# Performance work log

Hardware: AMD Instinct MI355X
Metric: run time of the kernel (lower is better)

## Reference

```python
import jax, jax.numpy as jnp
import numpy as np

N_NODES = 200_000
N_EDGES = 6_400_000
N_GRAPHS = 1024
F_IN = 16
H1 = 8
H2 = 16
STEPS = 4


def setup_inputs() -> dict:
    key = jax.random.key(0)
    ks = jax.random.split(key, 16)
    x = jax.random.normal(ks[0], (N_NODES, F_IN), jnp.float32)
    edge_index = jax.random.randint(ks[1], (2, N_EDGES), 0, N_NODES, dtype=jnp.int64)
    batch = jnp.sort(jax.random.randint(ks[2], (N_NODES,), 0, N_GRAPHS, dtype=jnp.int64))

    def p(k, shape):
        return jax.random.normal(k, shape, jnp.float32) * 0.1

    return {
        "x": x, "edge_index": edge_index, "batch": batch,
        # SAGEConv1: lin_l (neighbors, with bias) + lin_r (root, no bias)
        "W1l": p(ks[3], (H1, F_IN)), "b1l": jnp.zeros((H1,), jnp.float32), "W1r": p(ks[4], (H1, F_IN)),
        # SAGEConv2
        "W2l": p(ks[5], (H2, H1)), "b2l": jnp.zeros((H2,), jnp.float32), "W2r": p(ks[6], (H2, H1)),
        # Set2Set LSTM: input 2*H2, hidden H2, torch gate order (i, f, g, o)
        "Wih": p(ks[7], (4 * H2, 2 * H2)), "Whh": p(ks[8], (4 * H2, H2)),
        "bih": jnp.zeros((4 * H2,), jnp.float32), "bhh": jnp.zeros((4 * H2,), jnp.float32),
        # Final fc: 2*H2 -> 2
        "Wfc": p(ks[9], (2, 2 * H2)), "bfc": jnp.zeros((2,), jnp.float32),
    }


def _sage_conv(x, src, dst, Wl, bl, Wr):
    # PyG SAGEConv (mean aggr): out = lin_l(mean_j x_j) + lin_r(x_i)
    n = x.shape[0]
    agg = jax.ops.segment_sum(x[src], dst, num_segments=n)          # [N, F]
    deg = jax.ops.segment_sum(jnp.ones_like(dst, dtype=x.dtype), dst, num_segments=n)
    agg = agg / jnp.maximum(deg, 1.0)[:, None]
    return agg @ Wl.T + bl + x @ Wr.T


def _set2set(x, batch, Wih, Whh, bih, bhh):
    # order-invariant pooling with iterative content attention
    B = N_GRAPHS
    h = jnp.zeros((B, H2), x.dtype)
    c = jnp.zeros((B, H2), x.dtype)
    q_star = jnp.zeros((B, 2 * H2), x.dtype)
    for _ in range(STEPS):
        gates = q_star @ Wih.T + bih + h @ Whh.T + bhh
        i, f, g, o = jnp.split(gates, 4, axis=-1)
        c = jax.nn.sigmoid(f) * c + jax.nn.sigmoid(i) * jnp.tanh(g)
        h = jax.nn.sigmoid(o) * jnp.tanh(c)
        q = h                                                      # [B, H2]
        e = jnp.sum(x * q[batch], axis=-1)                         # [N]
        emax = jax.ops.segment_max(e, batch, num_segments=B)
        a = jnp.exp(e - emax[batch])
        asum = jax.ops.segment_sum(a, batch, num_segments=B)
        a = a / asum[batch]                                        # segment softmax
        r = jax.ops.segment_sum(a[:, None] * x, batch, num_segments=B)  # [B, H2]
        q_star = jnp.concatenate([q, r], axis=-1)
    return q_star


def reference(x, edge_index, batch, W1l, b1l, W1r, W2l, b2l, W2r,
              Wih, Whh, bih, bhh, Wfc, bfc):
    src, dst = edge_index[0], edge_index[1]
    x = jax.nn.relu(_sage_conv(x, src, dst, W1l, b1l, W1r))
    x = jax.nn.relu(_sage_conv(x, src, dst, W2l, b2l, W2r))
    q_star = _set2set(x, batch, Wih, Whh, bih, bhh)
    return q_star @ Wfc.T + bfc
```

## Files before the change

### kernel.cpp

```cpp
#include <hip/hip_runtime.h>

#define N_NODES 200000
#define N_EDGES 6400000
#define N_GRAPHS 1024
#define F_IN 16
#define H1 8
#define H2 16
#define STEPS 4

#define NB 1024
#define BNODES 196
#define NSLAB 8
#define CAPS 1024
#define BSLOTS (NSLAB * CAPS)
#define CAP 8784
#define SMAX 320
#define RPT 16
#define RPADD 200
#define ZIDX N_NODES

typedef _Float16 half8 __attribute__((ext_vector_type(8)));
typedef int int4v __attribute__((ext_vector_type(4)));

__global__ void k_y1(const float* __restrict__ x, const float* __restrict__ W1l,
                     _Float16* __restrict__ y1, _Float16* __restrict__ h1) {
    int n = blockIdx.x * blockDim.x + threadIdx.x;
    if (n > N_NODES) return;
    if (n == N_NODES) {
        half8 z = {};
        *(half8*)&y1[(long long)ZIDX * H1] = z;
        *(half8*)&h1[(long long)ZIDX * H1] = z;
        return;
    }
    float xv[F_IN];
#pragma unroll
    for (int k = 0; k < F_IN; k++) xv[k] = x[(long long)n * F_IN + k];
    half8 o;
#pragma unroll
    for (int j = 0; j < H1; j++) {
        float s = 0.f;
#pragma unroll
        for (int k = 0; k < F_IN; k++) s += W1l[j * F_IN + k] * xv[k];
        o[j] = (_Float16)s;
    }
    *(half8*)&y1[(long long)n * H1] = o;
}

#define FILL_T 16384
__global__ __launch_bounds__(1024) void k_bin_fill(const int* __restrict__ src,
                                                   const int* __restrict__ dst,
                                                   int* __restrict__ gcur8,
                                                   unsigned int* __restrict__ grec) {
    __shared__ int scnt[NB];
    __shared__ int soff[NB];
    int tid = threadIdx.x;
    int slab = blockIdx.x & (NSLAB - 1);
    long long ebase = (long long)blockIdx.x * FILL_T;
    scnt[tid] = 0;
    __syncthreads();
    unsigned int rec[16];
    unsigned int meta[16];
#pragma unroll
    for (int u = 0; u < 16; u++) {
        long long e = ebase + (long long)u * 1024 + tid;
        if (e < N_EDGES) {
            int d = __builtin_nontemporal_load(dst + e);
            int s = __builtin_nontemporal_load(src + e);
            int b = d / BNODES;
            int dl = d - b * BNODES;
            rec[u] = ((unsigned int)s << 8) | (unsigned int)dl;
            int r = atomicAdd(&scnt[b], 1);
            meta[u] = ((unsigned int)b << 16) | (unsigned int)r;
        } else {
            meta[u] = 0xFFFFFFFFu;
        }
    }
    __syncthreads();
    {
        int c = scnt[tid];
        soff[tid] = c ? atomicAdd(&gcur8[tid * NSLAB + slab], c) : 0;
    }
    __syncthreads();
#pragma unroll
    for (int u = 0; u < 16; u++) {
        if (meta[u] != 0xFFFFFFFFu) {
            int b = meta[u] >> 16;
            unsigned int slot = (unsigned int)soff[b] + (meta[u] & 0xFFFFu);
            if (slot < CAPS)
                grec[(size_t)b * BSLOTS + slab * CAPS + slot] = rec[u];
        }
    }
}

__global__ __launch_bounds__(512) void k_conv1(
    const float* __restrict__ x, const _Float16* __restrict__ y1,
    const int* __restrict__ gcur8, unsigned int* __restrict__ grec,
    int* __restrict__ growptr,
    const float* __restrict__ b1l, const float* __restrict__ W1r,
    _Float16* __restrict__ h1) {
    __shared__ __align__(16) int lsrc[CAP];
    __shared__ int hist[BNODES];
    __shared__ int start[BNODES + 1];
    __shared__ int slen[BNODES];
    __shared__ int wsum[8];
    __shared__ int cnt8[NSLAB];
    int b = blockIdx.x, tid = threadIdx.x;
    size_t base = (size_t)b * BSLOTS;
    if (tid < NSLAB) {
        int c = gcur8[b * NSLAB + tid];
        cnt8[tid] = c > CAPS ? CAPS : c;
    }
    for (int j = tid; j < BNODES; j += 512) hist[j] = 0;
    __syncthreads();
    unsigned int rec[RPT];
#pragma unroll
    for (int u = 0; u < RPT; u++) {
        int idx = u * 512 + tid;
        int s = idx >> 10, slot = idx & (CAPS - 1);
        if (slot < cnt8[s]) {
            rec[u] = __builtin_nontemporal_load(grec + base + idx);
            atomicAdd(&hist[rec[u] & 255], 1);
        } else {
            rec[u] = 0xFFFFFFFFu;
        }
    }
    __syncthreads();
    {
        int v = (tid < BNODES) ? hist[tid] : 0;
        int pl = (v + 3) & ~3;
        int lane = tid & 63, w = tid >> 6;
        int s = pl;
#pragma unroll
        for (int off = 1; off < 64; off <<= 1) {
            int u = __shfl_up(s, off);
            if (lane >= off) s += u;
        }
        if (lane == 63) wsum[w] = s;
        __syncthreads();
        int bb = 0;
        for (int i = 0; i < w; i++) bb += wsum[i];
        s += bb;
        int ps = s - pl;
        if (tid < BNODES) {
            start[tid] = ps; slen[tid] = v;
            growptr[b * RPADD + tid] = (ps << 16) | v;
        }
        if (tid == BNODES) {
            start[tid] = ps;
            growptr[b * RPADD + tid] = (ps << 16);
        }
    }
    __syncthreads();
    int ptotal = start[BNODES];
    for (int j = tid; j < BNODES; j += 512) hist[j] = 0;
    for (int j = tid; j < ptotal; j += 512) lsrc[j] = ZIDX;
    __syncthreads();
#pragma unroll
    for (int u = 0; u < RPT; u++) {
        if (rec[u] != 0xFFFFFFFFu) {
            int dl = rec[u] & 255;
            int k = atomicAdd(&hist[dl], 1);
            lsrc[start[dl] + k] = (int)(rec[u] >> 8);
        }
    }
    __syncthreads();
    {
        int pe = ptotal > BSLOTS ? BSLOTS : ptotal;
        for (int j = tid * 4; j < pe; j += 2048) {
            int4v vv = *(const int4v*)&lsrc[j];
            __builtin_nontemporal_store(vv, (int4v*)(grec + base + j));
        }
    }
    if (tid < 2 * BNODES) {
        int dl = tid >> 1, half = tid & 1;
        int n = b * BNODES + dl;
        int ps0 = start[dl];
        int nblk = (start[dl + 1] - ps0) >> 2;
        int c0 = half ? (nblk >> 1) : 0;
        int c1 = half ? nblk : (nblk >> 1);
        float acc[H1];
#pragma unroll
        for (int k = 0; k < H1; k++) acc[k] = 0.f;
        for (int blk = c0; blk < c1; blk++) {
            int4v a = *(const int4v*)&lsrc[ps0 + 4 * blk];
            half8 v0 = *(const half8*)&y1[(long long)a.x * H1];
            half8 v1 = *(const half8*)&y1[(long long)a.y * H1];
            half8 v2 = *(const half8*)&y1[(long long)a.z * H1];
            half8 v3 = *(const half8*)&y1[(long long)a.w * H1];
#pragma unroll
            for (int k = 0; k < H1; k++)
                acc[k] += ((float)v0[k] + (float)v1[k]) + ((float)v2[k] + (float)v3[k]);
        }
#pragma unroll
        for (int k = 0; k < H1; k++) acc[k] += __shfl_xor(acc[k], 1);
        if (half == 0 && n < N_NODES) {
            float inv = 1.0f / fmaxf((float)slen[dl], 1.0f);
            float xv[F_IN];
#pragma unroll
            for (int k = 0; k < F_IN; k++) xv[k] = x[(long long)n * F_IN + k];
            half8 o;
#pragma unroll
            for (int j = 0; j < H1; j++) {
                float s = acc[j] * inv + b1l[j];
#pragma unroll
                for (int k = 0; k < F_IN; k++) s += W1r[j * F_IN + k] * xv[k];
                o[j] = (_Float16)fmaxf(s, 0.0f);
            }
            *(half8*)&h1[(long long)n * H1] = o;
        }
    }
}

__global__ __launch_bounds__(512) void k_conv2(
    const _Float16* __restrict__ h1,
    const unsigned int* __restrict__ gsorted, const int* __restrict__ growptr,
    const float* __restrict__ b2l, const float* __restrict__ W2l,
    const float* __restrict__ W2r, float* __restrict__ h2) {
    int b = blockIdx.x, tid = threadIdx.x;
    if (tid >= 2 * BNODES) return;
    int dl = tid >> 1, half = tid & 1;
    int n = b * BNODES + dl;
    if (n >= N_NODES) return;
    int pack0 = growptr[b * RPADD + dl];
    int pack1 = growptr[b * RPADD + dl + 1];
    int ps0 = pack0 >> 16, sl = pack0 & 0xFFFF;
    int nblk = ((pack1 >> 16) - ps0) >> 2;
    const int4v* seg4 = (const int4v*)(gsorted + (size_t)b * BSLOTS + ps0);
    int c0 = half ? (nblk >> 1) : 0;
    int c1 = half ? nblk : (nblk >> 1);
    float acc[H1];
#pragma unroll
    for (int k = 0; k < H1; k++) acc[k] = 0.f;
    for (int blk = c0; blk < c1; blk++) {
        int4v a = __builtin_nontemporal_load(seg4 + blk);
        half8 v0 = *(const half8*)&h1[(long long)a.x * H1];
        half8 v1 = *(const half8*)&h1[(long long)a.y * H1];
        half8 v2 = *(const half8*)&h1[(long long)a.z * H1];
        half8 v3 = *(const half8*)&h1[(long long)a.w * H1];
#pragma unroll
        for (int k = 0; k < H1; k++)
            acc[k] += ((float)v0[k] + (float)v1[k]) + ((float)v2[k] + (float)v3[k]);
    }
#pragma unroll
    for (int k = 0; k < H1; k++) acc[k] += __shfl_xor(acc[k], 1);
    if (half == 0) {
        float inv = 1.0f / fmaxf((float)sl, 1.0f);
        float av[H1], hv[H1];
        half8 hr = *(const half8*)&h1[(long long)n * H1];
#pragma unroll
        for (int k = 0; k < H1; k++) { hv[k] = (float)hr[k]; av[k] = acc[k] * inv; }
        float o[H2];
#pragma unroll
        for (int j = 0; j < H2; j++) {
            float s = b2l[j];
#pragma unroll
            for (int k = 0; k < H1; k++) s += W2l[j * H1 + k] * av[k] + W2r[j * H1 + k] * hv[k];
            o[j] = fmaxf(s, 0.0f);
        }
        *(float4*)&h2[(long long)n * H2] = make_float4(o[0], o[1], o[2], o[3]);
        *(float4*)&h2[(long long)n * H2 + 4] = make_float4(o[4], o[5], o[6], o[7]);
        *(float4*)&h2[(long long)n * H2 + 8] = make_float4(o[8], o[9], o[10], o[11]);
        *(float4*)&h2[(long long)n * H2 + 12] = make_float4(o[12], o[13], o[14], o[15]);
    }
}

__global__ void k_ptr(const int* __restrict__ batch, int* __restrict__ ptr) {
    int n = blockIdx.x * blockDim.x + threadIdx.x;
    if (n >= N_NODES) return;
    int b = batch[n];
    int bp = (n == 0) ? -1 : batch[n - 1];
    for (int g = bp + 1; g <= b; g++) ptr[g] = n;
    if (n == N_NODES - 1) {
        for (int g = b + 1; g <= N_GRAPHS; g++) ptr[g] = N_NODES;
    }
}

__global__ __launch_bounds__(256) void k_set2set(
    const float* __restrict__ h2, const int* __restrict__ ptr,
    const float* __restrict__ Wih, const float* __restrict__ Whh,
    const float* __restrict__ bih, const float* __restrict__ bhh,
    const float* __restrict__ Wfc, const float* __restrict__ bfc,
    float* __restrict__ out) {
    int b = blockIdx.x;
    int start = ptr[b], end = ptr[b + 1], cnt = end - start;
    __shared__ float sx[SMAX][H2 + 1];
    __shared__ float el[SMAX];
    __shared__ float sh[H2], sc[H2], sq[2 * H2], sg[4 * H2];
    __shared__ float red[4][17];
    __shared__ float s_emax, s_asum, s_r[H2];
    int tid = threadIdx.x;
    int wid = tid >> 6, lane = tid & 63;
    bool fit = (cnt <= SMAX);

    if (fit) {
        for (int i = start + tid; i < end; i += 256) {
            const float4* p = (const float4*)&h2[(long long)i * H2];
            float4 r0 = p[0], r1 = p[1], r2 = p[2], r3 = p[3];
            float* row = sx[i - start];
            row[0] = r0.x; row[1] = r0.y; row[2] = r0.z; row[3] = r0.w;
            row[4] = r1.x; row[5] = r1.y; row[6] = r1.z; row[7] = r1.w;
            row[8] = r2.x; row[9] = r2.y; row[10] = r2.z; row[11] = r2.w;
            row[12] = r3.x; row[13] = r3.y; row[14] = r3.z; row[15] = r3.w;
        }
    }
    if (tid < H2) { sh[tid] = 0.f; sc[tid] = 0.f; }
    if (tid < 2 * H2) sq[tid] = 0.f;
    __syncthreads();

    for (int step = 0; step < STEPS; step++) {
        if (tid < 64) {
            float g = bih[tid] + bhh[tid];
#pragma unroll
            for (int k = 0; k < 2 * H2; k++) g += Wih[tid * (2 * H2) + k] * sq[k];
#pragma unroll
            for (int k = 0; k < H2; k++) g += Whh[tid * H2 + k] * sh[k];
            sg[tid] = g;
        }
        __syncthreads();
        if (tid < H2) {
            float ig = 1.f / (1.f + expf(-sg[tid]));
            float fg = 1.f / (1.f + expf(-sg[H2 + tid]));
            float gg = tanhf(sg[2 * H2 + tid]);
            float og = 1.f / (1.f + expf(-sg[3 * H2 + tid]));
            float cc = fg * sc[tid] + ig * gg;
            sc[tid] = cc;
            sh[tid] = og * tanhf(cc);
        }
        __syncthreads();

        float lmax = -3.0e38f;
        if (fit) {
            for (int ii = tid; ii < cnt; ii += 256) {
                float e = 0.f;
#pragma unroll
                for (int k = 0; k < H2; k++) e += sx[ii][k] * sh[k];
                el[ii] = e;
                lmax = fmaxf(lmax, e);
            }
        } else {
            for (int i = start + tid; i < end; i += 256) {
                float e = 0.f;
#pragma unroll
                for (int k = 0; k < H2; k++) e += h2[(long long)i * H2 + k] * sh[k];
                lmax = fmaxf(lmax, e);
            }
        }
        for (int off = 32; off; off >>= 1) lmax = fmaxf(lmax, __shfl_down(lmax, off));
        if (lane == 0) red[wid][0] = lmax;
        __syncthreads();
        if (tid == 0) {
            float m = red[0][0];
            for (int w = 1; w < 4; w++) m = fmaxf(m, red[w][0]);
            s_emax = m;
        }
        __syncthreads();
        float emax = s_emax;

        float asum = 0.f, rloc[H2];
#pragma unroll
        for (int k = 0; k < H2; k++) rloc[k] = 0.f;
        if (fit) {
            for (int ii = tid; ii < cnt; ii += 256) {
                float a = expf(el[ii] - emax);
                asum += a;
#pragma unroll
                for (int k = 0; k < H2; k++) rloc[k] += a * sx[ii][k];
            }
        } else {
            for (int i = start + tid; i < end; i += 256) {
                float hv[H2];
                float e = 0.f;
#pragma unroll
                for (int k = 0; k < H2; k++) { hv[k] = h2[(long long)i * H2 + k]; e += hv[k] * sh[k]; }
                float a = expf(e - emax);
                asum += a;
#pragma unroll
                for (int k = 0; k < H2; k++) rloc[k] += a * hv[k];
            }
        }
        for (int off = 32; off; off >>= 1) {
            asum += __shfl_down(asum, off);
#pragma unroll
            for (int k = 0; k < H2; k++) rloc[k] += __shfl_down(rloc[k], off);
        }
        if (lane == 0) {
            red[wid][16] = asum;
#pragma unroll
            for (int k = 0; k < H2; k++) red[wid][k] = rloc[k];
        }
        __syncthreads();
        if (tid < 17) {
            float s = red[0][tid] + red[1][tid] + red[2][tid] + red[3][tid];
            if (tid == 16) s_asum = s; else s_r[tid] = s;
        }
        __syncthreads();
        if (tid < H2) {
            float rr = (cnt > 0 && s_asum > 0.f) ? s_r[tid] / s_asum : 0.0f;
            sq[tid] = sh[tid];
            sq[H2 + tid] = rr;
        }
        __syncthreads();
    }

    if (tid < 2) {
        float s = bfc[tid];
#pragma unroll
        for (int k = 0; k < 2 * H2; k++) s += Wfc[tid * (2 * H2) + k] * sq[k];
        out[b * 2 + tid] = s;
    }
}

extern "C" void kernel_launch(void* const* d_in, const int* in_sizes, int n_in,
                              void* d_out, int out_size, void* d_ws, size_t ws_size,
                              hipStream_t stream) {
    const float* x   = (const float*)d_in[0];
    const int*   ei  = (const int*)d_in[1];
    const int*   src = ei;
    const int*   dst = ei + N_EDGES;
    const int*   batch = (const int*)d_in[2];
    const float* W1l = (const float*)d_in[3];
    const float* b1l = (const float*)d_in[4];
    const float* W1r = (const float*)d_in[5];
    const float* W2l = (const float*)d_in[6];
    const float* b2l = (const float*)d_in[7];
    const float* W2r = (const float*)d_in[8];
    const float* Wih = (const float*)d_in[9];
    const float* Whh = (const float*)d_in[10];
    const float* bih = (const float*)d_in[11];
    const float* bhh = (const float*)d_in[12];
    const float* Wfc = (const float*)d_in[13];
    const float* bfc = (const float*)d_in[14];
    float* out = (float*)d_out;

    char* ws = (char*)d_ws;
    unsigned int* grec = (unsigned int*)ws;
    int* gcur8 = (int*)(grec + (size_t)NB * BSLOTS);
    int* growptr = gcur8 + NB * NSLAB;
    _Float16* y1 = (_Float16*)(growptr + (size_t)NB * RPADD);
    _Float16* h1 = y1 + (size_t)(N_NODES + 4) * H1;
    float* h2  = (float*)(h1 + (size_t)(N_NODES + 4) * H1);
    int*   ptr = (int*)(h2 + (size_t)N_NODES * H2);

    hipMemsetAsync(gcur8, 0, (size_t)NB * NSLAB * sizeof(int), stream);

    int nb_node1 = (N_NODES + 1 + 255) / 256;
    int nb_node = (N_NODES + 255) / 256;
    int nb_fill = (int)(((long long)N_EDGES + FILL_T - 1) / FILL_T);

    k_y1<<<nb_node1, 256, 0, stream>>>(x, W1l, y1, h1);
    k_bin_fill<<<nb_fill, 1024, 0, stream>>>(src, dst, gcur8, grec);
    k_conv1<<<NB, 512, 0, stream>>>(x, y1, gcur8, grec, growptr, b1l, W1r, h1);
    k_conv2<<<NB, 512, 0, stream>>>(h1, grec, growptr, b2l, W2l, W2r, h2);
    k_ptr<<<nb_node, 256, 0, stream>>>(batch, ptr);
    k_set2set<<<N_GRAPHS, 256, 0, stream>>>(h2, ptr, Wih, Whh, bih, bhh, Wfc, bfc, out);
}
```

Measured before the change: 201.0 us.

## Gather neighbors with 32 lanes per node in both SAGE conv kernels

Replaces the two-threads-per-node neighbor gather in conv1 and conv2 with a half-wavefront of 32 lanes per destination node that strides over its edges and reduces with xor shuffles. Each lane then computes one output feature. conv2 is relaunched with 8 nodes per 256-thread block instead of one bin per block. The aim is more memory-level parallelism and load balance for the random gathers, at the cost of extra shuffle reductions and idle lanes on low-degree nodes.

```diff
diff --git a/kernel.cpp b/kernel.cpp
--- a/kernel.cpp
+++ b/kernel.cpp
@@ -171,96 +171,73 @@
             __builtin_nontemporal_store(vv, (int4v*)(grec + base + j));
         }
     }
-    if (tid < 2 * BNODES) {
-        int dl = tid >> 1, half = tid & 1;
+    int gid = tid >> 5, l = tid & 31;
+    for (int dl = gid; dl < BNODES; dl += 16) {
         int n = b * BNODES + dl;
-        int ps0 = start[dl];
-        int nblk = (start[dl + 1] - ps0) >> 2;
-        int c0 = half ? (nblk >> 1) : 0;
-        int c1 = half ? nblk : (nblk >> 1);
+        int ps0 = start[dl], pe = start[dl + 1];
         float acc[H1];
 #pragma unroll
         for (int k = 0; k < H1; k++) acc[k] = 0.f;
-        for (int blk = c0; blk < c1; blk++) {
-            int4v a = *(const int4v*)&lsrc[ps0 + 4 * blk];
-            half8 v0 = *(const half8*)&y1[(long long)a.x * H1];
-            half8 v1 = *(const half8*)&y1[(long long)a.y * H1];
-            half8 v2 = *(const half8*)&y1[(long long)a.z * H1];
-            half8 v3 = *(const half8*)&y1[(long long)a.w * H1];
-#pragma unroll
-            for (int k = 0; k < H1; k++)
-                acc[k] += ((float)v0[k] + (float)v1[k]) + ((float)v2[k] + (float)v3[k]);
-        }
-#pragma unroll
-        for (int k = 0; k < H1; k++) acc[k] += __shfl_xor(acc[k], 1);
-        if (half == 0 && n < N_NODES) {
+        for (int e = ps0 + l; e < pe; e += 32) {
+            half8 v = *(const half8*)&y1[(long long)lsrc[e] * H1];
+#pragma unroll
+            for (int k = 0; k < H1; k++) acc[k] += (float)v[k];
+        }
+#pragma unroll
+        for (int off = 16; off; off >>= 1) {
+#pragma unroll
+            for (int k = 0; k < H1; k++) acc[k] += __shfl_xor(acc[k], off);
+        }
+        if (l < H1 && n < N_NODES) {
+            float aj = acc[0];
+#pragma unroll
+            for (int k = 1; k < H1; k++) if (l == k) aj = acc[k];
             float inv = 1.0f / fmaxf((float)slen[dl], 1.0f);
-            float xv[F_IN];
-#pragma unroll
-            for (int k = 0; k < F_IN; k++) xv[k] = x[(long long)n * F_IN + k];
-            half8 o;
-#pragma unroll
-            for (int j = 0; j < H1; j++) {
-                float s = acc[j] * inv + b1l[j];
-#pragma unroll
-                for (int k = 0; k < F_IN; k++) s += W1r[j * F_IN + k] * xv[k];
-                o[j] = (_Float16)fmaxf(s, 0.0f);
-            }
-            *(half8*)&h1[(long long)n * H1] = o;
-        }
-    }
-}
-
-__global__ __launch_bounds__(512) void k_conv2(
+            float s = aj * inv + b1l[l];
+#pragma unroll
+            for (int k = 0; k < F_IN; k++) s += W1r[l * F_IN + k] * x[(long long)n * F_IN + k];
+            h1[(long long)n * H1 + l] = (_Float16)fmaxf(s, 0.0f);
+        }
+    }
+}
+
+__global__ __launch_bounds__(256) void k_conv2(
     const _Float16* __restrict__ h1,
     const unsigned int* __restrict__ gsorted, const int* __restrict__ growptr,
     const float* __restrict__ b2l, const float* __restrict__ W2l,
     const float* __restrict__ W2r, float* __restrict__ h2) {
-    int b = blockIdx.x, tid = threadIdx.x;
-    if (tid >= 2 * BNODES) return;
-    int dl = tid >> 1, half = tid & 1;
-    int n = b * BNODES + dl;
+    int tid = threadIdx.x;
+    int gid = tid >> 5, l = tid & 31;
+    int n = blockIdx.x * 8 + gid;
     if (n >= N_NODES) return;
+    int b = n / BNODES, dl = n - b * BNODES;
     int pack0 = growptr[b * RPADD + dl];
     int pack1 = growptr[b * RPADD + dl + 1];
     int ps0 = pack0 >> 16, sl = pack0 & 0xFFFF;
-    int nblk = ((pack1 >> 16) - ps0) >> 2;
-    const int4v* seg4 = (const int4v*)(gsorted + (size_t)b * BSLOTS + ps0);
-    int c0 = half ? (nblk >> 1) : 0;
-    int c1 = half ? nblk : (nblk >> 1);
+    int pe = pack1 >> 16;
+    const unsigned int* seg = gsorted + (size_t)b * BSLOTS;
     float acc[H1];
 #pragma unroll
     for (int k = 0; k < H1; k++) acc[k] = 0.f;
-    for (int blk = c0; blk < c1; blk++) {
-        int4v a = __builtin_nontemporal_load(seg4 + blk);
-        half8 v0 = *(const half8*)&h1[(long long)a.x * H1];
-        half8 v1 = *(const half8*)&h1[(long long)a.y * H1];
-        half8 v2 = *(const half8*)&h1[(long long)a.z * H1];
-        half8 v3 = *(const half8*)&h1[(long long)a.w * H1];
+    for (int e = ps0 + l; e < pe; e += 32) {
+        int idx = (int)__builtin_nontemporal_load(seg + e);
+        half8 v = *(const half8*)&h1[(long long)idx * H1];
+#pragma unroll
+        for (int k = 0; k < H1; k++) acc[k] += (float)v[k];
+    }
+#pragma unroll
+    for (int off = 16; off; off >>= 1) {
+#pragma unroll
+        for (int k = 0; k < H1; k++) acc[k] += __shfl_xor(acc[k], off);
+    }
+    if (l < H2) {
+        float inv = 1.0f / fmaxf((float)sl, 1.0f);
+        half8 hr = *(const half8*)&h1[(long long)n * H1];
+        float s = b2l[l];
 #pragma unroll
         for (int k = 0; k < H1; k++)
-            acc[k] += ((float)v0[k] + (float)v1[k]) + ((float)v2[k] + (float)v3[k]);
-    }
-#pragma unroll
-    for (int k = 0; k < H1; k++) acc[k] += __shfl_xor(acc[k], 1);
-    if (half == 0) {
-        float inv = 1.0f / fmaxf((float)sl, 1.0f);
-        float av[H1], hv[H1];
-        half8 hr = *(const half8*)&h1[(long long)n * H1];
-#pragma unroll
-        for (int k = 0; k < H1; k++) { hv[k] = (float)hr[k]; av[k] = acc[k] * inv; }
-        float o[H2];
-#pragma unroll
-        for (int j = 0; j < H2; j++) {
-            float s = b2l[j];
-#pragma unroll
-            for (int k = 0; k < H1; k++) s += W2l[j * H1 + k] * av[k] + W2r[j * H1 + k] * hv[k];
-            o[j] = fmaxf(s, 0.0f);
-        }
-        *(float4*)&h2[(long long)n * H2] = make_float4(o[0], o[1], o[2], o[3]);
-        *(float4*)&h2[(long long)n * H2 + 4] = make_float4(o[4], o[5], o[6], o[7]);
-        *(float4*)&h2[(long long)n * H2 + 8] = make_float4(o[8], o[9], o[10], o[11]);
-        *(float4*)&h2[(long long)n * H2 + 12] = make_float4(o[12], o[13], o[14], o[15]);
+            s += W2l[l * H1 + k] * (acc[k] * inv) + W2r[l * H1 + k] * (float)hr[k];
+        h2[(long long)n * H2 + l] = fmaxf(s, 0.0f);
     }
 }
 
@@ -446,11 +423,12 @@
     int nb_node1 = (N_NODES + 1 + 255) / 256;
     int nb_node = (N_NODES + 255) / 256;
     int nb_fill = (int)(((long long)N_EDGES + FILL_T - 1) / FILL_T);
+    int nb_conv2 = (N_NODES + 7) / 8;
 
     k_y1<<<nb_node1, 256, 0, stream>>>(x, W1l, y1, h1);
     k_bin_fill<<<nb_fill, 1024, 0, stream>>>(src, dst, gcur8, grec);
     k_conv1<<<NB, 512, 0, stream>>>(x, y1, gcur8, grec, growptr, b1l, W1r, h1);
-    k_conv2<<<NB, 512, 0, stream>>>(h1, grec, growptr, b2l, W2l, W2r, h2);
+    k_conv2<<<nb_conv2, 256, 0, stream>>>(h1, grec, growptr, b2l, W2l, W2r, h2);
     k_ptr<<<nb_node, 256, 0, stream>>>(batch, ptr);
     k_set2set<<<N_GRAPHS, 256, 0, stream>>>(h2, ptr, Wih, Whh, bih, bhh, Wfc, bfc, out);
 }
```

Result: slower. 223.0 us (+11.0%).
